# Performance work log

Measured on AMD Instinct MI355X. Metric: run time of the kernel, lower is better.

## Reference

```python
import jax, jax.numpy as jnp
import numpy as np

S = 1000          # support size = n_way * k_shot
FEAT = 640        # feat_dim
LAT = 64          # latent_dim
REL = 2 * LAT     # relation_dim = 128
NWAY = 20


def setup_inputs() -> dict:
    key = jax.random.key(0)
    ks = jax.random.split(key, 5)
    scale = 1.0 / np.sqrt(FEAT)
    return {
        "support": jax.random.normal(ks[0], (S, FEAT), dtype=jnp.float32),
        "W_enc": jax.random.normal(ks[1], (LAT, FEAT), dtype=jnp.float32) * scale,
        "W1": jax.random.normal(ks[2], (REL, REL), dtype=jnp.float32) * (1.0 / np.sqrt(REL)),
        "W2": jax.random.normal(ks[3], (REL, REL), dtype=jnp.float32) * (1.0 / np.sqrt(REL)),
        "W3": jax.random.normal(ks[4], (REL, REL), dtype=jnp.float32) * (1.0 / np.sqrt(REL)),
        "n_way": NWAY,
    }


def reference(support, W_enc, W1, W2, W3, n_way):
    s = support.shape[0]
    # encoder: bias-free linear  [S, LAT]
    emb = support @ W_enc.T
    # prepare_for_rel_net: all-pairs concat, row i*S+j = [emb[i], emb[j]]
    left = jnp.repeat(emb, s, axis=0)          # [S*S, LAT]
    right = jnp.tile(emb, (s, 1))              # [S*S, LAT]
    cat = jnp.concatenate([left, right], axis=1)  # [S*S, 2*LAT]
    # relation_net: three bias-free linears, no activations
    rel = ((cat @ W1.T) @ W2.T) @ W3.T         # [S*S, REL]
    # view(n_way, -1, S, REL).mean(dim=2)
    outputs = rel.reshape(n_way, -1, s, rel.shape[-1]).mean(axis=2)  # [n_way, k_shot, REL]
    # average_codes_per_class: mean over shots, expanded back
    codes = jnp.broadcast_to(outputs.mean(axis=1, keepdims=True), outputs.shape)
    return codes
```

## Files before the change

### kernel.cpp

```cpp
#include <hip/hip_runtime.h>

#define FEAT 640
#define LAT 64
#define REL 128
#define NWAY 20
#define KSHOT 50
#define PARTS 5
#define RPP (KSHOT / PARTS)
#define NPROD (NWAY * PARTS)
#define OUT_FLOATS (NWAY * KSHOT * REL)
#define MAGIC 0x5EED1234u
#define WS_NEED ((size_t)(NPROD * LAT) * sizeof(float) + NPROD * sizeof(unsigned))

__global__ __launch_bounds__(1024) void leo_onepass(const float* __restrict__ support,
                                                    const float* __restrict__ W_enc,
                                                    const float* __restrict__ W1,
                                                    const float* __restrict__ W2,
                                                    const float* __restrict__ W3,
                                                    float* __restrict__ out,
                                                    float* __restrict__ pemb,
                                                    unsigned* __restrict__ flags) {
    __shared__ float4 s_part[4][160];
    __shared__ float  s_cm[FEAT];
    __shared__ float  s_emb[NWAY * LAT];
    __shared__ float  s_v[4][REL];

    const int b = blockIdx.x;
    const int t = threadIdx.x;
    const int p = b / NWAY, c = b % NWAY;

    if (t < 640) {
        const int col4 = t % 160, rg = t / 160;
        const float4* base =
            (const float4*)(support + ((size_t)c * KSHOT + p * RPP) * FEAT) + col4;
        float4 a = make_float4(0.f, 0.f, 0.f, 0.f);
        for (int r = rg; r < RPP; r += 4) {
            const float4 v = base[(size_t)r * (FEAT / 4)];
            a.x += v.x; a.y += v.y; a.z += v.z; a.w += v.w;
        }
        s_part[rg][col4] = a;
    }
    __syncthreads();
    if (t < 160) {
        float4 a = s_part[0][t];
#pragma unroll
        for (int g = 1; g < 4; ++g) {
            const float4 v = s_part[g][t];
            a.x += v.x; a.y += v.y; a.z += v.z; a.w += v.w;
        }
        ((float4*)s_cm)[t] = a;
    }
    __syncthreads();

    {
        const int l = t >> 4, q = t & 15;
        const float4* wr = (const float4*)(W_enc + l * FEAT + q * 40);
        const float4* xv = (const float4*)(s_cm + q * 40);
        float a0 = 0.f, a1 = 0.f, a2 = 0.f, a3 = 0.f;
#pragma unroll
        for (int i = 0; i < 10; ++i) {
            const float4 w = wr[i], x = xv[i];
            a0 += w.x * x.x; a1 += w.y * x.y; a2 += w.z * x.z; a3 += w.w * x.w;
        }
        float acc = (a0 + a1) + (a2 + a3);
        acc += __shfl_xor(acc, 8, 16);
        acc += __shfl_xor(acc, 4, 16);
        acc += __shfl_xor(acc, 2, 16);
        acc += __shfl_xor(acc, 1, 16);
        if (q == 0) pemb[b * LAT + l] = acc * (1.0f / KSHOT);
    }
    __syncthreads();
    if (t == 0) {
        __threadfence();
        __hip_atomic_store(&flags[b], MAGIC, __ATOMIC_RELEASE, __HIP_MEMORY_SCOPE_AGENT);
    }

    if (b >= NWAY) return;

    if (t < NPROD) {
        while (__hip_atomic_load(&flags[t], __ATOMIC_ACQUIRE,
                                 __HIP_MEMORY_SCOPE_AGENT) != MAGIC) {
            __builtin_amdgcn_s_sleep(2);
        }
    }
    __syncthreads();

    for (int i = t; i < NWAY * LAT; i += 1024) {
        float s = 0.f;
#pragma unroll
        for (int q = 0; q < PARTS; ++q)
            s += __hip_atomic_load(&pemb[q * NWAY * LAT + i], __ATOMIC_RELAXED,
                                   __HIP_MEMORY_SCOPE_AGENT);
        s_emb[i] = s;
    }
    __syncthreads();

    if (t < LAT) {
        float s = 0.f;
#pragma unroll
        for (int cc = 0; cc < NWAY; ++cc) s += s_emb[cc * LAT + t];
        s_v[0][LAT + t] = s * (1.0f / NWAY);
    } else if (t < 2 * LAT) {
        s_v[0][t - LAT] = s_emb[c * LAT + (t - LAT)];
    }
    __syncthreads();

    auto stage = [&](const float* __restrict__ W, const float* sin_, float* sout) {
        const int r = t >> 3, q = t & 7;
        const float4* wr = (const float4*)(W + r * REL + q * 16);
        const float4* xv = (const float4*)(sin_ + q * 16);
        float a0 = 0.f, a1 = 0.f, a2 = 0.f, a3 = 0.f;
#pragma unroll
        for (int i = 0; i < 4; ++i) {
            const float4 w = wr[i], x = xv[i];
            a0 += w.x * x.x; a1 += w.y * x.y; a2 += w.z * x.z; a3 += w.w * x.w;
        }
        float acc = (a0 + a1) + (a2 + a3);
        acc += __shfl_xor(acc, 4, 8);
        acc += __shfl_xor(acc, 2, 8);
        acc += __shfl_xor(acc, 1, 8);
        if (q == 0) sout[r] = acc;
        __syncthreads();
    };
    stage(W1, s_v[0], s_v[1]);
    stage(W2, s_v[1], s_v[2]);
    stage(W3, s_v[2], s_v[3]);

    const float4* codes4 = (const float4*)s_v[3];
    float4* out4 = (float4*)out + (size_t)c * (KSHOT * REL / 4);
    for (int i = t; i < KSHOT * REL / 4; i += 1024) out4[i] = codes4[i & 31];
}

__global__ __launch_bounds__(1024) void leo_emb(const float* __restrict__ support,
                                                const float* __restrict__ W_enc,
                                                float* emb_ws) {
    __shared__ float4 s_part[6][160];
    __shared__ float  s_cm[FEAT];
    const int c = blockIdx.x, t = threadIdx.x;
    if (t < 960) {
        const int col4 = t % 160, rg = t / 160;
        const float4* base = (const float4*)(support + (size_t)c * KSHOT * FEAT) + col4;
        float4 a = make_float4(0.f, 0.f, 0.f, 0.f);
        for (int r = rg; r < KSHOT; r += 6) {
            const float4 v = base[(size_t)r * (FEAT / 4)];
            a.x += v.x; a.y += v.y; a.z += v.z; a.w += v.w;
        }
        s_part[rg][col4] = a;
    }
    __syncthreads();
    if (t < 160) {
        float4 a = s_part[0][t];
#pragma unroll
        for (int g = 1; g < 6; ++g) {
            const float4 v = s_part[g][t];
            a.x += v.x; a.y += v.y; a.z += v.z; a.w += v.w;
        }
        const float inv = 1.0f / KSHOT;
        ((float4*)s_cm)[t] = make_float4(a.x * inv, a.y * inv, a.z * inv, a.w * inv);
    }
    __syncthreads();
    const int l = t >> 4, q = t & 15;
    const float4* wr = (const float4*)(W_enc + l * FEAT + q * 40);
    const float4* xv = (const float4*)(s_cm + q * 40);
    float a0 = 0.f, a1 = 0.f, a2 = 0.f, a3 = 0.f;
#pragma unroll
    for (int i = 0; i < 10; ++i) {
        const float4 w = wr[i], x = xv[i];
        a0 += w.x * x.x; a1 += w.y * x.y; a2 += w.z * x.z; a3 += w.w * x.w;
    }
    float acc = (a0 + a1) + (a2 + a3);
    acc += __shfl_xor(acc, 8, 16);
    acc += __shfl_xor(acc, 4, 16);
    acc += __shfl_xor(acc, 2, 16);
    acc += __shfl_xor(acc, 1, 16);
    if (q == 0) emb_ws[c * LAT + l] = acc;
}

__global__ __launch_bounds__(1024) void leo_codes(const float* emb_ws,
                                                  const float* __restrict__ W1,
                                                  const float* __restrict__ W2,
                                                  const float* __restrict__ W3,
                                                  float* out, int skip_tail) {
    __shared__ float s_emb[NWAY * LAT];
    __shared__ float s_v[4][REL];
    const int c = blockIdx.x, t = threadIdx.x;
    for (int i = t; i < NWAY * LAT; i += 1024) s_emb[i] = emb_ws[i];
    __syncthreads();
    if (t < LAT) {
        float s = 0.f;
#pragma unroll
        for (int cc = 0; cc < NWAY; ++cc) s += s_emb[cc * LAT + t];
        s_v[0][LAT + t] = s * (1.0f / NWAY);
    } else if (t < 2 * LAT) {
        s_v[0][t - LAT] = s_emb[c * LAT + (t - LAT)];
    }
    __syncthreads();
    auto stage = [&](const float* __restrict__ W, const float* sin_, float* sout) {
        const int r = t >> 3, q = t & 7;
        const float4* wr = (const float4*)(W + r * REL + q * 16);
        const float4* xv = (const float4*)(sin_ + q * 16);
        float a0 = 0.f, a1 = 0.f, a2 = 0.f, a3 = 0.f;
#pragma unroll
        for (int i = 0; i < 4; ++i) {
            const float4 w = wr[i], x = xv[i];
            a0 += w.x * x.x; a1 += w.y * x.y; a2 += w.z * x.z; a3 += w.w * x.w;
        }
        float acc = (a0 + a1) + (a2 + a3);
        acc += __shfl_xor(acc, 4, 8);
        acc += __shfl_xor(acc, 2, 8);
        acc += __shfl_xor(acc, 1, 8);
        if (q == 0) sout[r] = acc;
        __syncthreads();
    };
    stage(W1, s_v[0], s_v[1]);
    stage(W2, s_v[1], s_v[2]);
    stage(W3, s_v[2], s_v[3]);
    const float4* codes4 = (const float4*)s_v[3];
    float4* out4 = (float4*)out + (size_t)c * (KSHOT * REL / 4);
    const int n4 = (skip_tail && c == NWAY - 1) ? 40 * (REL / 4) : KSHOT * (REL / 4);
    for (int i = t; i < n4; i += 1024) out4[i] = codes4[i & 31];
}

__global__ __launch_bounds__(256) void leo_patch(float* out) {
    const int t = threadIdx.x;
    const float4* src = (const float4*)(out + (size_t)(NWAY - 1) * KSHOT * REL);
    float4* dst = (float4*)(out + ((size_t)(NWAY - 1) * KSHOT + 40) * REL);
    for (int i = t; i < 10 * (REL / 4); i += 256) dst[i] = src[i & 31];
}

extern "C" void kernel_launch(void* const* d_in, const int* in_sizes, int n_in,
                              void* d_out, int out_size, void* d_ws, size_t ws_size,
                              hipStream_t stream) {
    const float* support = (const float*)d_in[0];
    const float* W_enc   = (const float*)d_in[1];
    const float* W1      = (const float*)d_in[2];
    const float* W2      = (const float*)d_in[3];
    const float* W3      = (const float*)d_in[4];
    float* out = (float*)d_out;

    if (ws_size >= WS_NEED) {
        float* pemb = (float*)d_ws;
        unsigned* flags = (unsigned*)((char*)d_ws + (size_t)NPROD * LAT * sizeof(float));
        leo_onepass<<<NPROD, 1024, 0, stream>>>(support, W_enc, W1, W2, W3,
                                                out, pemb, flags);
    } else {
        float* emb_ws = out + OUT_FLOATS - NWAY * LAT;
        leo_emb  <<<NWAY, 1024, 0, stream>>>(support, W_enc, emb_ws);
        leo_codes<<<NWAY, 1024, 0, stream>>>(emb_ws, W1, W2, W3, out, 1);
        leo_patch<<<1, 256, 0, stream>>>(out);
    }
}
```

Measured before the change: 16.77 us.

## Let every producer block compute relation codes and write its own output slice

Every one of the 100 blocks now waits for all partial embeddings, recomputes the three relation-net matvecs redundantly, and writes only its 10-row slice of the output. Before, 20 blocks each wrote 50 rows. The per-element atomic loads of partial embeddings become plain loads behind a single agent-scope acquire fence, and the explicit threadfence before the release store is dropped. The fallback path is also switched to 100-way partial embedding with a larger patched tail. In exchange, all blocks spin-wait and repeat the small matvec chain.

```diff
diff --git a/kernel.cpp b/kernel.cpp
--- a/kernel.cpp
+++ b/kernel.cpp
@@ -9,7 +9,7 @@
 #define RPP (KSHOT / PARTS)
 #define NPROD (NWAY * PARTS)
 #define OUT_FLOATS (NWAY * KSHOT * REL)
-#define MAGIC 0x5EED1234u
+#define MAGIC 0x5EEDC0DEu
 #define WS_NEED ((size_t)(NPROD * LAT) * sizeof(float) + NPROD * sizeof(unsigned))
 
 __global__ __launch_bounds__(1024) void leo_onepass(const float* __restrict__ support,
@@ -70,12 +70,8 @@
         if (q == 0) pemb[b * LAT + l] = acc * (1.0f / KSHOT);
     }
     __syncthreads();
-    if (t == 0) {
-        __threadfence();
+    if (t == 0)
         __hip_atomic_store(&flags[b], MAGIC, __ATOMIC_RELEASE, __HIP_MEMORY_SCOPE_AGENT);
-    }
-
-    if (b >= NWAY) return;
 
     if (t < NPROD) {
         while (__hip_atomic_load(&flags[t], __ATOMIC_ACQUIRE,
@@ -84,13 +80,12 @@
         }
     }
     __syncthreads();
+    __builtin_amdgcn_fence(__ATOMIC_ACQUIRE, "agent");
 
     for (int i = t; i < NWAY * LAT; i += 1024) {
         float s = 0.f;
 #pragma unroll
-        for (int q = 0; q < PARTS; ++q)
-            s += __hip_atomic_load(&pemb[q * NWAY * LAT + i], __ATOMIC_RELAXED,
-                                   __HIP_MEMORY_SCOPE_AGENT);
+        for (int q = 0; q < PARTS; ++q) s += pemb[q * NWAY * LAT + i];
         s_emb[i] = s;
     }
     __syncthreads();
@@ -127,21 +122,23 @@
     stage(W3, s_v[2], s_v[3]);
 
     const float4* codes4 = (const float4*)s_v[3];
-    float4* out4 = (float4*)out + (size_t)c * (KSHOT * REL / 4);
-    for (int i = t; i < KSHOT * REL / 4; i += 1024) out4[i] = codes4[i & 31];
-}
-
-__global__ __launch_bounds__(1024) void leo_emb(const float* __restrict__ support,
-                                                const float* __restrict__ W_enc,
-                                                float* emb_ws) {
-    __shared__ float4 s_part[6][160];
+    float4* out4 = (float4*)out + ((size_t)c * KSHOT + p * RPP) * (REL / 4);
+    if (t < RPP * (REL / 4)) out4[t] = codes4[t & 31];
+}
+
+__global__ __launch_bounds__(1024) void leo_pemb(const float* __restrict__ support,
+                                                 const float* __restrict__ W_enc,
+                                                 float* __restrict__ pemb) {
+    __shared__ float4 s_part[4][160];
     __shared__ float  s_cm[FEAT];
-    const int c = blockIdx.x, t = threadIdx.x;
-    if (t < 960) {
+    const int b = blockIdx.x, t = threadIdx.x;
+    const int p = b / NWAY, c = b % NWAY;
+    if (t < 640) {
         const int col4 = t % 160, rg = t / 160;
-        const float4* base = (const float4*)(support + (size_t)c * KSHOT * FEAT) + col4;
+        const float4* base =
+            (const float4*)(support + ((size_t)c * KSHOT + p * RPP) * FEAT) + col4;
         float4 a = make_float4(0.f, 0.f, 0.f, 0.f);
-        for (int r = rg; r < KSHOT; r += 6) {
+        for (int r = rg; r < RPP; r += 4) {
             const float4 v = base[(size_t)r * (FEAT / 4)];
             a.x += v.x; a.y += v.y; a.z += v.z; a.w += v.w;
         }
@@ -151,12 +148,11 @@
     if (t < 160) {
         float4 a = s_part[0][t];
 #pragma unroll
-        for (int g = 1; g < 6; ++g) {
+        for (int g = 1; g < 4; ++g) {
             const float4 v = s_part[g][t];
             a.x += v.x; a.y += v.y; a.z += v.z; a.w += v.w;
         }
-        const float inv = 1.0f / KSHOT;
-        ((float4*)s_cm)[t] = make_float4(a.x * inv, a.y * inv, a.z * inv, a.w * inv);
+        ((float4*)s_cm)[t] = a;
     }
     __syncthreads();
     const int l = t >> 4, q = t & 15;
@@ -173,10 +169,10 @@
     acc += __shfl_xor(acc, 4, 16);
     acc += __shfl_xor(acc, 2, 16);
     acc += __shfl_xor(acc, 1, 16);
-    if (q == 0) emb_ws[c * LAT + l] = acc;
-}
-
-__global__ __launch_bounds__(1024) void leo_codes(const float* emb_ws,
+    if (q == 0) pemb[b * LAT + l] = acc * (1.0f / KSHOT);
+}
+
+__global__ __launch_bounds__(1024) void leo_codes(const float* pemb,
                                                   const float* __restrict__ W1,
                                                   const float* __restrict__ W2,
                                                   const float* __restrict__ W3,
@@ -184,7 +180,12 @@
     __shared__ float s_emb[NWAY * LAT];
     __shared__ float s_v[4][REL];
     const int c = blockIdx.x, t = threadIdx.x;
-    for (int i = t; i < NWAY * LAT; i += 1024) s_emb[i] = emb_ws[i];
+    for (int i = t; i < NWAY * LAT; i += 1024) {
+        float s = 0.f;
+#pragma unroll
+        for (int q = 0; q < PARTS; ++q) s += pemb[q * NWAY * LAT + i];
+        s_emb[i] = s;
+    }
     __syncthreads();
     if (t < LAT) {
         float s = 0.f;
@@ -217,15 +218,15 @@
     stage(W3, s_v[2], s_v[3]);
     const float4* codes4 = (const float4*)s_v[3];
     float4* out4 = (float4*)out + (size_t)c * (KSHOT * REL / 4);
-    const int n4 = (skip_tail && c == NWAY - 1) ? 40 * (REL / 4) : KSHOT * (REL / 4);
+    const int n4 = (skip_tail && c == NWAY - 1) ? 30 * (REL / 4) : KSHOT * (REL / 4);
     for (int i = t; i < n4; i += 1024) out4[i] = codes4[i & 31];
 }
 
 __global__ __launch_bounds__(256) void leo_patch(float* out) {
     const int t = threadIdx.x;
     const float4* src = (const float4*)(out + (size_t)(NWAY - 1) * KSHOT * REL);
-    float4* dst = (float4*)(out + ((size_t)(NWAY - 1) * KSHOT + 40) * REL);
-    for (int i = t; i < 10 * (REL / 4); i += 256) dst[i] = src[i & 31];
+    float4* dst = (float4*)(out + ((size_t)(NWAY - 1) * KSHOT + 30) * REL);
+    for (int i = t; i < 20 * (REL / 4); i += 256) dst[i] = src[i & 31];
 }
 
 extern "C" void kernel_launch(void* const* d_in, const int* in_sizes, int n_in,
@@ -244,9 +245,9 @@
         leo_onepass<<<NPROD, 1024, 0, stream>>>(support, W_enc, W1, W2, W3,
                                                 out, pemb, flags);
     } else {
-        float* emb_ws = out + OUT_FLOATS - NWAY * LAT;
-        leo_emb  <<<NWAY, 1024, 0, stream>>>(support, W_enc, emb_ws);
-        leo_codes<<<NWAY, 1024, 0, stream>>>(emb_ws, W1, W2, W3, out, 1);
+        float* pemb = out + OUT_FLOATS - NPROD * LAT;
+        leo_pemb <<<NPROD, 1024, 0, stream>>>(support, W_enc, pemb);
+        leo_codes<<<NWAY, 1024, 0, stream>>>(pemb, W1, W2, W3, out, 1);
         leo_patch<<<1, 256, 0, stream>>>(out);
     }
 }
```

Measured after the change: 29.14 us. +73.8%, slower.
